# Kernel optimization log

Measured on AMD Instinct MI355X. Metric: run time of the kernel, lower is better.

The kernel has to match this reference:

```python
import jax, jax.numpy as jnp
import numpy as np

N = 40000      # input points
M = 40000      # output points
E = 500000     # flat neighbor edges (ragged flattened)
F = 32         # input feature channels
C = 64         # output channels
K = 15         # kernel points
EXTENT = 0.6


def _make_kernel_points(k, radius):
    # Deterministic stand-in for load_kernels(): first point fixed at center,
    # remaining points spread inside a ball of the given radius.
    rng = np.random.RandomState(0)
    pts = rng.randn(k, 3).astype(np.float32)
    pts /= np.linalg.norm(pts, axis=1, keepdims=True) + 1e-9
    scale = rng.rand(k, 1).astype(np.float32) ** (1.0 / 3.0)
    pts = pts * scale * radius
    pts[0] = 0.0  # fixed='center'
    return jnp.asarray(pts)


def setup_inputs() -> dict:
    key = jax.random.key(0)
    ks = jax.random.split(key, 6)
    points = jax.random.uniform(ks[0], (N, 3), dtype=jnp.float32)
    features = jax.random.normal(ks[1], (N, F), dtype=jnp.float32)
    output_points = jax.random.uniform(ks[2], (M, 3), dtype=jnp.float32)
    neighbor_indices = jax.random.randint(ks[3], (E,), 0, N, dtype=jnp.int32)
    segment_ids = jnp.sort(jax.random.randint(ks[4], (E,), 0, M, dtype=jnp.int32))
    k_points = _make_kernel_points(K, 1.5 * EXTENT)          # [K,3] constant
    k_values = jax.random.normal(ks[5], (K, F, C), dtype=jnp.float32) * 0.05
    return {
        "points": points,
        "features": features,
        "output_points": output_points,
        "neighbor_indices": neighbor_indices,
        "segment_ids": segment_ids,
        "k_points": k_points,
        "k_values": k_values,
    }


def reference(points, features, output_points, neighbor_indices, segment_ids,
              k_points, k_values):
    # Gather neighbor coords/features and recenter around each output point.
    rel = points[neighbor_indices] - output_points[segment_ids]      # [E,3]
    nbr_feat = features[neighbor_indices]                            # [E,F]

    # Per-kernel-point squared distances and linear influence weights.
    diff = rel[:, None, :] - k_points[None, :, :]                    # [E,K,3]
    sq_dist = jnp.sum(diff * diff, axis=-1)                          # [E,K]
    w = jnp.maximum(1.0 - jnp.sqrt(sq_dist) / EXTENT, 0.0)           # [E,K]

    # Weighted features and ragged segment-sum per output point.
    weighted = w[:, :, None] * nbr_feat[:, None, :]                  # [E,K,F]
    agg = jax.ops.segment_sum(weighted, segment_ids, num_segments=M,
                              indices_are_sorted=True)               # [M,K,F]

    # Batched matmul over kernel points, then sum over kernel points.
    out = jnp.einsum('mkf,kfc->mc', agg, k_values)                   # [M,C]
    return out
```

## Files before the change

kernel.cpp:

```cpp
#include <hip/hip_runtime.h>

typedef __attribute__((ext_vector_type(8))) short bf16x8;
typedef __attribute__((ext_vector_type(8))) _Float16 f16x8;
typedef __attribute__((ext_vector_type(4))) float f32x4;
typedef __attribute__((ext_vector_type(4))) _Float16 f16x4;
typedef __attribute__((ext_vector_type(2))) _Float16 f16x2;

#define NPTS   40000
#define MOUT   40000
#define EDG    500000
#define FIN    32
#define COUT   64
#define KP     15
#define KFDIM  (KP * FIN)
#define EXTENT 0.6f

#define FSTRIDE 112
#define WSTRIDE 40
#define WAVE_LDS (16 * FSTRIDE + 16 * WSTRIDE)
#define ASTR 488

#define FEAT_BLKS  (NPTS * FIN / 1024)
#define PTS_BLKS   ((NPTS + 255) / 256)
#define OP_BLKS    ((MOUT + 255) / 256)
#define ROW_BLKS   ((EDG + 255) / 256)
#define WT_BLKS    (KFDIM * COUT / 256)
#define PRE_BLKS   (FEAT_BLKS + PTS_BLKS + OP_BLKS + ROW_BLKS + WT_BLKS)

__device__ __forceinline__ short f2bf(float x) {
    union { float f; unsigned u; } v; v.f = x;
    unsigned r = (v.u + 0x7fffu + ((v.u >> 16) & 1u)) >> 16;
    return (short)r;
}

__global__ __launch_bounds__(256) void preprocess_all(
    const float* __restrict__ features, _Float16* __restrict__ feat_i,
    const float* __restrict__ pts, float4* __restrict__ p4,
    const float* __restrict__ opts, float4* __restrict__ op4,
    const int* __restrict__ seg_ids, int* __restrict__ row_start,
    const float* __restrict__ k_values, _Float16* __restrict__ w_t)
{
    const int bid = blockIdx.x;
    if (bid < FEAT_BLKS) {
        const int d0 = (bid * 256 + threadIdx.x) * 4;
        #pragma unroll
        for (int u = 0; u < 4; ++u) {
            const int d = d0 + u;
            const int p = d >> 5, q = d & 31;
            const int fp = q >> 1, h = q & 1;
            feat_i[d] = (_Float16)features[p * FIN + fp + 16 * h];
        }
    } else if (bid < FEAT_BLKS + PTS_BLKS) {
        const int i = (bid - FEAT_BLKS) * 256 + threadIdx.x;
        if (i < NPTS) {
            const float* p = pts + 3 * i;
            p4[i] = make_float4(p[0], p[1], p[2], 0.f);
        }
    } else if (bid < FEAT_BLKS + PTS_BLKS + OP_BLKS) {
        const int i = (bid - FEAT_BLKS - PTS_BLKS) * 256 + threadIdx.x;
        if (i < MOUT) {
            const float* p = opts + 3 * i;
            op4[i] = make_float4(p[0], p[1], p[2], 0.f);
        }
    } else if (bid < FEAT_BLKS + PTS_BLKS + OP_BLKS + ROW_BLKS) {
        const int e = (bid - FEAT_BLKS - PTS_BLKS - OP_BLKS) * 256 + threadIdx.x;
        if (e >= EDG) return;
        const int cur  = seg_ids[e];
        const int prev = (e == 0) ? -1 : seg_ids[e - 1];
        for (int m = prev + 1; m <= cur; ++m) row_start[m] = e;
        if (e == EDG - 1)
            for (int m = cur + 1; m <= MOUT; ++m) row_start[m] = EDG;
    } else {
        const int d = (bid - FEAT_BLKS - PTS_BLKS - OP_BLKS - ROW_BLKS) * 256
                      + threadIdx.x;
        const int c = d / KFDIM, r = d % KFDIM;
        const int k = r >> 5, q = r & 31;
        const int fp = q >> 1, h = q & 1;
        w_t[d] = (_Float16)k_values[(k * FIN + fp + 16 * h) * COUT + c];
    }
}

__global__ __launch_bounds__(256, 5) void kpconv_fused2(
    const float4* __restrict__ points4,
    const _Float16* __restrict__ feat_i,
    const float4* __restrict__ op4,
    const int*   __restrict__ nbr_idx,
    const int*   __restrict__ row_start,
    const float* __restrict__ k_points,
    const _Float16* __restrict__ w_t,
    float* __restrict__ out)
{
    __shared__ __align__(16) _Float16 aggT[16 * ASTR];
    __shared__ __align__(16) unsigned char stage[4 * WAVE_LDS];

    const int tid  = threadIdx.x;
    const int wave = tid >> 6;
    const int lane = tid & 63;
    const int quad = lane >> 4;
    const int l16  = lane & 15;
    const int esl  = lane >> 2;
    const int kg   = lane & 3;
    const int m0   = blockIdx.x * 16;

    unsigned char* fbase = stage + wave * WAVE_LDS;
    unsigned char* wbase = fbase + 16 * FSTRIDE;

    float kx[4], ky[4], kz[4];
    #pragma unroll
    for (int t = 0; t < 4; ++t) {
        const int k  = kg * 4 + t;
        const int kk = k < KP ? k : 0;
        kx[t] = k_points[kk * 3 + 0];
        ky[t] = k_points[kk * 3 + 1];
        kz[t] = k_points[kk * 3 + 2];
    }
    const float inv_ext = 1.f / EXTENT;

    int rs[5];
    #pragma unroll
    for (int i = 0; i < 5; ++i) rs[i] = row_start[m0 + wave * 4 + i];

    int nstart[4];
    nstart[3] = rs[4];
    nstart[2] = (rs[3] < rs[4]) ? rs[3] : rs[4];
    nstart[1] = (rs[2] < rs[3]) ? rs[2] : nstart[2];
    nstart[0] = (rs[1] < rs[2]) ? rs[1] : nstart[1];
    const int fstart = (rs[0] < rs[1]) ? rs[0] : nstart[0];

    int wb = -0x40000000;
    int nbrreg = 0;
    uint4  fc_n = {0, 0, 0, 0};
    float4 p_n  = make_float4(0.f, 0.f, 0.f, 0.f);

    auto pref = [&](int es) {
        if (es + 15 > wb + 63) {
            wb = es;
            const int a = wb + lane;
            nbrreg = nbr_idx[a < EDG ? a : EDG - 1];
        }
        const int e  = es + esl;
        const int nb = __shfl(nbrreg, e - wb);
        fc_n = *(const uint4*)(feat_i + nb * FIN + kg * 8);
        p_n  = ((const float4*)points4)[nb];
    };

    pref(fstart);

    #pragma unroll
    for (int j = 0; j < 4; ++j) {
        const int e0 = rs[j];
        const int e1 = rs[j + 1];
        const float4 o = op4[m0 + wave * 4 + j];

        f32x4 c_lo = {0.f, 0.f, 0.f, 0.f};
        f32x4 c_hi = {0.f, 0.f, 0.f, 0.f};

        for (int es = e0; es < e1; es += 16) {
            const uint4  fc = fc_n;
            const float4 p  = p_n;
            const int nes = (es + 16 < e1) ? es + 16 : nstart[j];
            pref(nes);

            *(uint4*)(fbase + esl * FSTRIDE + kg * 16) = fc;

            const float rx = p.x - o.x, ry = p.y - o.y, rz = p.z - o.z;
            const bool evalid = (es + esl) < e1;
            #pragma unroll
            for (int t = 0; t < 4; ++t) {
                const float dx = rx - kx[t], dy = ry - ky[t], dz = rz - kz[t];
                float w = 1.f - sqrtf(dx * dx + dy * dy + dz * dz) * inv_ext;
                w = w > 0.f ? w : 0.f;
                if (!evalid || (kg * 4 + t) >= KP) w = 0.f;
                *(_Float16*)(wbase + (kg * 4 + t) * WSTRIDE + esl * 2) = (_Float16)w;
            }

            const f16x4 af = *(const f16x4*)(wbase + l16 * WSTRIDE + quad * 8);
            f16x2 w2[4];
            #pragma unroll
            for (int jj = 0; jj < 4; ++jj)
                w2[jj] = *(const f16x2*)(fbase + (quad * 4 + jj) * FSTRIDE + l16 * 4);
            const f16x4 blo = {w2[0][0], w2[1][0], w2[2][0], w2[3][0]};
            const f16x4 bhi = {w2[0][1], w2[1][1], w2[2][1], w2[3][1]};

            c_lo = __builtin_amdgcn_mfma_f32_16x16x16f16(af, blo, c_lo, 0, 0, 0);
            c_hi = __builtin_amdgcn_mfma_f32_16x16x16f16(af, bhi, c_hi, 0, 0, 0);
        }

        _Float16* dst = aggT + (wave * 4 + j) * ASTR;
        #pragma unroll
        for (int r = 0; r < 4; ++r) {
            const int krow = quad * 4 + r;
            if (krow < KP) {
                f16x2 v = {(_Float16)c_lo[r], (_Float16)c_hi[r]};
                *(f16x2*)(dst + krow * 32 + 2 * l16) = v;
            }
        }
    }

    __syncthreads();

    const int bcol = wave * 16 + l16;
    const _Float16* wrow = w_t + (size_t)bcol * KFDIM + quad * 8;
    const _Float16* arow = aggT + l16 * ASTR + quad * 8;

    f32x4 c = {0.f, 0.f, 0.f, 0.f};
    #pragma unroll
    for (int s = 0; s < 15; ++s) {
        const f16x8 a = *(const f16x8*)(arow + 32 * s);
        const f16x8 b = *(const f16x8*)(wrow + 32 * s);
        c = __builtin_amdgcn_mfma_f32_16x16x32_f16(a, b, c, 0, 0, 0);
    }

    #pragma unroll
    for (int r = 0; r < 4; ++r)
        out[(m0 + quad * 4 + r) * COUT + bcol] = c[r];
}

__global__ __launch_bounds__(256, 4) void kpconv_agg_fallback(
    const float* __restrict__ points,
    const float* __restrict__ features,
    const float* __restrict__ output_points,
    const int*   __restrict__ nbr_idx,
    const int*   __restrict__ seg_ids,
    const float* __restrict__ k_points,
    _Float16* __restrict__ agg_g)
{
    __shared__ int seg_start[5];

    const int tid = threadIdx.x;
    const int m0  = blockIdx.x * 4;

    if (tid <= 4) {
        const int target = m0 + tid;
        int lo = 0, hi = EDG;
        while (lo < hi) {
            int mid = (lo + hi) >> 1;
            if (seg_ids[mid] < target) lo = mid + 1; else hi = mid;
        }
        seg_start[tid] = lo;
    }
    __syncthreads();

    const int wave = tid >> 6;
    const int lane = tid & 63;
    const int quad = lane >> 4;
    const int l16  = lane & 15;

    const int m = m0 + wave;
    const float ox = output_points[m * 3 + 0];
    const float oy = output_points[m * 3 + 1];
    const float oz = output_points[m * 3 + 2];

    const int myk = l16 < KP ? l16 : 0;
    const float kpx = k_points[myk * 3 + 0];
    const float kpy = k_points[myk * 3 + 1];
    const float kpz = k_points[myk * 3 + 2];
    const float inv_ext = 1.f / EXTENT;

    const int e0 = seg_start[wave], e1 = seg_start[wave + 1];

    f32x4 c_lo = {0.f, 0.f, 0.f, 0.f};
    f32x4 c_hi = {0.f, 0.f, 0.f, 0.f};

    for (int es = e0; es < e1; es += 32) {
        const int last = e1 - 1;
        const int ebase = es + quad * 8;

        int nb[8];
        #pragma unroll
        for (int j = 0; j < 8; ++j) {
            const int e = ebase + j;
            nb[j] = nbr_idx[e < e1 ? e : last];
        }

        bf16x8 afrag, blo, bhi;
        #pragma unroll
        for (int j = 0; j < 8; ++j) {
            const float* pp = points + nb[j] * 3;
            const float rx = pp[0] - ox;
            const float ry = pp[1] - oy;
            const float rz = pp[2] - oz;
            const float dx = rx - kpx, dy = ry - kpy, dz = rz - kpz;
            const float d2 = dx * dx + dy * dy + dz * dz;
            float w = 1.f - sqrtf(d2) * inv_ext;
            w = w > 0.f ? w : 0.f;
            if (l16 >= KP || ebase + j >= e1) w = 0.f;
            afrag[j] = f2bf(w);
        }

        #pragma unroll
        for (int j = 0; j < 8; ++j) {
            const float* fp = features + nb[j] * FIN + l16;
            blo[j] = f2bf(fp[0]);
            bhi[j] = f2bf(fp[16]);
        }

        c_lo = __builtin_amdgcn_mfma_f32_16x16x32_bf16(afrag, blo, c_lo, 0, 0, 0);
        c_hi = __builtin_amdgcn_mfma_f32_16x16x32_bf16(afrag, bhi, c_hi, 0, 0, 0);
    }

    _Float16* dst = agg_g + (size_t)m * KFDIM;
    #pragma unroll
    for (int r = 0; r < 4; ++r) {
        const int krow = quad * 4 + r;
        if (krow < KP) {
            dst[krow * FIN + l16]      = (_Float16)c_lo[r];
            dst[krow * FIN + 16 + l16] = (_Float16)c_hi[r];
        }
    }
}

__global__ __launch_bounds__(256, 4) void kpconv_gemm_plain(
    const _Float16* __restrict__ agg_g,
    const float* __restrict__ k_values,
    float* __restrict__ out)
{
    const int tid  = threadIdx.x;
    const int wave = tid >> 6;
    const int lane = tid & 63;
    const int quad = lane >> 4;
    const int l16  = lane & 15;
    const int m0   = blockIdx.x * 32;
    const int bcol = wave * 16 + l16;

    f16x8 bfr[15];
    #pragma unroll
    for (int s = 0; s < 15; ++s) {
        #pragma unroll
        for (int j = 0; j < 8; ++j)
            bfr[s][j] = (_Float16)k_values[(32 * s + quad * 8 + j) * COUT + bcol];
    }

    const _Float16* arow0 = agg_g + (size_t)(m0 + l16) * KFDIM + quad * 8;
    const _Float16* arow1 = arow0 + 16 * KFDIM;

    f32x4 c0 = {0.f, 0.f, 0.f, 0.f};
    f32x4 c1 = {0.f, 0.f, 0.f, 0.f};
    #pragma unroll
    for (int s = 0; s < 15; ++s) {
        const f16x8 a0 = *(const f16x8*)(arow0 + 32 * s);
        const f16x8 a1 = *(const f16x8*)(arow1 + 32 * s);
        c0 = __builtin_amdgcn_mfma_f32_16x16x32_f16(a0, bfr[s], c0, 0, 0, 0);
        c1 = __builtin_amdgcn_mfma_f32_16x16x32_f16(a1, bfr[s], c1, 0, 0, 0);
    }

    #pragma unroll
    for (int r = 0; r < 4; ++r) {
        out[(m0 + quad * 4 + r) * COUT + bcol]      = c0[r];
        out[(m0 + 16 + quad * 4 + r) * COUT + bcol] = c1[r];
    }
}

extern "C" void kernel_launch(void* const* d_in, const int* in_sizes, int n_in,
                              void* d_out, int out_size, void* d_ws, size_t ws_size,
                              hipStream_t stream) {
    const float* points        = (const float*)d_in[0];
    const float* features      = (const float*)d_in[1];
    const float* output_points = (const float*)d_in[2];
    const int*   nbr_idx       = (const int*)d_in[3];
    const int*   seg_ids       = (const int*)d_in[4];
    const float* k_points      = (const float*)d_in[5];
    const float* k_values      = (const float*)d_in[6];
    float* out = (float*)d_out;

    const size_t feat_bytes = (size_t)NPTS * FIN * sizeof(_Float16);
    const size_t pts4_bytes = (size_t)NPTS * sizeof(float4);
    const size_t op4_bytes  = (size_t)MOUT * sizeof(float4);
    const size_t rs_bytes   = ((size_t)(MOUT + 1) * sizeof(int) + 15) & ~15ul;
    const size_t wt_bytes   = (size_t)KFDIM * COUT * sizeof(_Float16);
    const size_t full_bytes = feat_bytes + pts4_bytes + op4_bytes + rs_bytes
                            + wt_bytes;

    if (ws_size >= full_bytes) {
        char* p = (char*)d_ws;
        _Float16* feat_i    = (_Float16*)p;  p += feat_bytes;
        float4*   points4   = (float4*)p;    p += pts4_bytes;
        float4*   op4       = (float4*)p;    p += op4_bytes;
        int*      row_start = (int*)p;       p += rs_bytes;
        _Float16* w_t       = (_Float16*)p;

        preprocess_all<<<PRE_BLKS, 256, 0, stream>>>(
            features, feat_i, points, points4, output_points, op4,
            seg_ids, row_start, k_values, w_t);
        kpconv_fused2<<<MOUT / 16, 256, 0, stream>>>(
            points4, feat_i, op4, nbr_idx, row_start, k_points, w_t, out);
    } else {
        _Float16* agg_g = (_Float16*)d_ws;
        kpconv_agg_fallback<<<MOUT / 4, 256, 0, stream>>>(
            points, features, output_points, nbr_idx, seg_ids, k_points, agg_g);
        kpconv_gemm_plain<<<MOUT / 32, 256, 0, stream>>>(agg_g, k_values, out);
    }
}
```

Before: 101.9 us.

## Build MFMA operands directly in registers instead of staging through LDS

Each lane now gathers the four edges' point coordinates and its own feature pair straight into the registers that form the MFMA A and B operands, computing the kernel-point weight for its own kernel row. This removes the per-wave LDS staging buffers, the LDS writes and reads, and the implicit wave-level dependency each chunk. In exchange each lane issues four scattered 4-byte feature loads and four float4 point loads per chunk instead of one 16-byte feature load. It also computes four sqrt weights per lane, with redundant point loads across lanes.

```diff
diff --git a/kernel.cpp b/kernel.cpp
--- a/kernel.cpp
+++ b/kernel.cpp
@@ -15,9 +15,6 @@
 #define KFDIM  (KP * FIN)
 #define EXTENT 0.6f
 
-#define FSTRIDE 112
-#define WSTRIDE 40
-#define WAVE_LDS (16 * FSTRIDE + 16 * WSTRIDE)
 #define ASTR 488
 
 #define FEAT_BLKS  (NPTS * FIN / 1024)
@@ -91,29 +88,19 @@
     float* __restrict__ out)
 {
     __shared__ __align__(16) _Float16 aggT[16 * ASTR];
-    __shared__ __align__(16) unsigned char stage[4 * WAVE_LDS];
 
     const int tid  = threadIdx.x;
     const int wave = tid >> 6;
     const int lane = tid & 63;
     const int quad = lane >> 4;
     const int l16  = lane & 15;
-    const int esl  = lane >> 2;
-    const int kg   = lane & 3;
     const int m0   = blockIdx.x * 16;
 
-    unsigned char* fbase = stage + wave * WAVE_LDS;
-    unsigned char* wbase = fbase + 16 * FSTRIDE;
-
-    float kx[4], ky[4], kz[4];
-    #pragma unroll
-    for (int t = 0; t < 4; ++t) {
-        const int k  = kg * 4 + t;
-        const int kk = k < KP ? k : 0;
-        kx[t] = k_points[kk * 3 + 0];
-        ky[t] = k_points[kk * 3 + 1];
-        kz[t] = k_points[kk * 3 + 2];
-    }
+    const int  myk = l16 < KP ? l16 : 0;
+    const float kxx = k_points[myk * 3 + 0];
+    const float kyy = k_points[myk * 3 + 1];
+    const float kzz = k_points[myk * 3 + 2];
+    const bool  vk  = (l16 < KP);
     const float inv_ext = 1.f / EXTENT;
 
     int rs[5];
@@ -129,8 +116,9 @@
 
     int wb = -0x40000000;
     int nbrreg = 0;
-    uint4  fc_n = {0, 0, 0, 0};
-    float4 p_n  = make_float4(0.f, 0.f, 0.f, 0.f);
+    float4 p0n, p1n, p2n, p3n;
+    unsigned f0n = 0, f1n = 0, f2n = 0, f3n = 0;
+    p0n = p1n = p2n = p3n = make_float4(0.f, 0.f, 0.f, 0.f);
 
     auto pref = [&](int es) {
         if (es + 15 > wb + 63) {
@@ -138,10 +126,19 @@
             const int a = wb + lane;
             nbrreg = nbr_idx[a < EDG ? a : EDG - 1];
         }
-        const int e  = es + esl;
-        const int nb = __shfl(nbrreg, e - wb);
-        fc_n = *(const uint4*)(feat_i + nb * FIN + kg * 8);
-        p_n  = ((const float4*)points4)[nb];
+        const int base = es - wb + quad * 4;
+        const int n0 = __shfl(nbrreg, base + 0);
+        const int n1 = __shfl(nbrreg, base + 1);
+        const int n2 = __shfl(nbrreg, base + 2);
+        const int n3 = __shfl(nbrreg, base + 3);
+        p0n = points4[n0];
+        p1n = points4[n1];
+        p2n = points4[n2];
+        p3n = points4[n3];
+        f0n = *(const unsigned*)(feat_i + n0 * FIN + 2 * l16);
+        f1n = *(const unsigned*)(feat_i + n1 * FIN + 2 * l16);
+        f2n = *(const unsigned*)(feat_i + n2 * FIN + 2 * l16);
+        f3n = *(const unsigned*)(feat_i + n3 * FIN + 2 * l16);
     };
 
     pref(fstart);
@@ -156,31 +153,31 @@
         f32x4 c_hi = {0.f, 0.f, 0.f, 0.f};
 
         for (int es = e0; es < e1; es += 16) {
-            const uint4  fc = fc_n;
-            const float4 p  = p_n;
+            const float4  P0 = p0n, P1 = p1n, P2 = p2n, P3 = p3n;
+            const unsigned F0 = f0n, F1 = f1n, F2 = f2n, F3 = f3n;
             const int nes = (es + 16 < e1) ? es + 16 : nstart[j];
             pref(nes);
 
-            *(uint4*)(fbase + esl * FSTRIDE + kg * 16) = fc;
-
-            const float rx = p.x - o.x, ry = p.y - o.y, rz = p.z - o.z;
-            const bool evalid = (es + esl) < e1;
-            #pragma unroll
-            for (int t = 0; t < 4; ++t) {
-                const float dx = rx - kx[t], dy = ry - ky[t], dz = rz - kz[t];
-                float w = 1.f - sqrtf(dx * dx + dy * dy + dz * dz) * inv_ext;
-                w = w > 0.f ? w : 0.f;
-                if (!evalid || (kg * 4 + t) >= KP) w = 0.f;
-                *(_Float16*)(wbase + (kg * 4 + t) * WSTRIDE + esl * 2) = (_Float16)w;
+            f16x4 af;
+#define EDGE_W(jj, Pj)                                                        \
+            {                                                                 \
+                const float rx = Pj.x - o.x, ry = Pj.y - o.y, rz = Pj.z - o.z;\
+                const float dx = rx - kxx, dy = ry - kyy, dz = rz - kzz;      \
+                float w = 1.f - sqrtf(dx*dx + dy*dy + dz*dz) * inv_ext;       \
+                w = w > 0.f ? w : 0.f;                                        \
+                if (!vk || (es + quad * 4 + jj) >= e1) w = 0.f;               \
+                af[jj] = (_Float16)w;                                         \
             }
-
-            const f16x4 af = *(const f16x4*)(wbase + l16 * WSTRIDE + quad * 8);
-            f16x2 w2[4];
-            #pragma unroll
-            for (int jj = 0; jj < 4; ++jj)
-                w2[jj] = *(const f16x2*)(fbase + (quad * 4 + jj) * FSTRIDE + l16 * 4);
-            const f16x4 blo = {w2[0][0], w2[1][0], w2[2][0], w2[3][0]};
-            const f16x4 bhi = {w2[0][1], w2[1][1], w2[2][1], w2[3][1]};
+            EDGE_W(0, P0)
+            EDGE_W(1, P1)
+            EDGE_W(2, P2)
+            EDGE_W(3, P3)
+#undef EDGE_W
+
+            union { unsigned u; f16x2 h; } U0, U1, U2, U3;
+            U0.u = F0; U1.u = F1; U2.u = F2; U3.u = F3;
+            const f16x4 blo = {U0.h[0], U1.h[0], U2.h[0], U3.h[0]};
+            const f16x4 bhi = {U0.h[1], U1.h[1], U2.h[1], U3.h[1]};
 
             c_lo = __builtin_amdgcn_mfma_f32_16x16x16f16(af, blo, c_lo, 0, 0, 0);
             c_hi = __builtin_amdgcn_mfma_f32_16x16x16f16(af, bhi, c_hi, 0, 0, 0);
```

New measurement: 104.2 us. 1.02x slower.
